# Performance work log

Measured on AMD Instinct MI355X. Metric: run time of the kernel, lower is better.

## Reference

```python
import jax, jax.numpy as jnp
import numpy as np

B, S, D, H = 4, 4096, 1024, 16
DK = D // H  # 64


def setup_inputs() -> dict:
    key = jax.random.key(0)
    ks = jax.random.split(key, 8)
    scale = 1.0 / np.sqrt(D)
    return {
        "query": jax.random.normal(ks[0], (B, S, D), dtype=jnp.float32),
        "key": jax.random.normal(ks[1], (B, S, D), dtype=jnp.float32),
        "value": jax.random.normal(ks[2], (B, S, D), dtype=jnp.float32),
        "Wq": jax.random.normal(ks[3], (D, D), dtype=jnp.float32) * scale,
        "Wk": jax.random.normal(ks[4], (D, D), dtype=jnp.float32) * scale,
        "Wv": jax.random.normal(ks[5], (D, D), dtype=jnp.float32) * scale,
        "Wo": jax.random.normal(ks[6], (D, D), dtype=jnp.float32) * scale,
        "bo": jnp.zeros((D,), dtype=jnp.float32),
    }


def _phi(x):
    # ELU + 1 feature map
    return jax.nn.elu(x) + 1.0


def _heads(x, W):
    # torch Linear: y = x @ W.T; then [B,S,D] -> [B,H,S,DK]
    y = jnp.einsum("bsd,ed->bse", x, W)
    return y.reshape(x.shape[0], x.shape[1], H, DK).transpose(0, 2, 1, 3)


def reference(query, key, value, Wq, Wk, Wv, Wo, bo):
    Q = _phi(_heads(query, Wq))   # [B,H,Sq,DK]
    K = _phi(_heads(key, Wk))     # [B,H,Sk,DK]
    V = _heads(value, Wv)         # [B,H,Sk,DK]

    KV = jnp.einsum("bhsd,bhse->bhde", K, V)        # [B,H,DK,DK]
    num = jnp.einsum("bhqd,bhde->bhqe", Q, KV)       # [B,H,Sq,DK]
    den = jnp.einsum("bhqd,bhd->bhq", Q, K.sum(axis=2))  # [B,H,Sq]
    out = num / (den[..., None] + 1e-6)

    out = out.transpose(0, 2, 1, 3).reshape(query.shape[0], query.shape[1], D)
    return jnp.einsum("bsd,ed->bse", out, Wo) + bo
```

## Files before the change

kernel.cpp:

```cpp
#include <hip/hip_runtime.h>


typedef unsigned short ushort_t;
typedef __bf16 bf16x8 __attribute__((ext_vector_type(8)));
typedef float f32x4 __attribute__((ext_vector_type(4)));
typedef void gvoid_t __attribute__((address_space(1)));
typedef void svoid_t __attribute__((address_space(3)));

#define BB 4
#define SS 4096
#define DD 1024
#define HH 16
#define DKk 64
#define MM (BB * SS)

__device__ __forceinline__ ushort_t f2bf(float f) {
  unsigned int u = __float_as_uint(f);
  u += 0x7fffu + ((u >> 16) & 1u);
  return (ushort_t)(u >> 16);
}
__device__ __forceinline__ float b2f(ushort_t h) {
  return __uint_as_float(((unsigned int)h) << 16);
}
__device__ __forceinline__ void gld_lds16(const ushort_t* g, ushort_t* l) {
  __builtin_amdgcn_global_load_lds((gvoid_t*)g, (svoid_t*)l, 16, 0, 0);
}
__device__ __forceinline__ bf16x8 ldfrag(const ushort_t* p) {
  return *(const bf16x8*)p;
}

__global__ __launch_bounds__(256) void cast3_kernel(
    const float* __restrict__ q, const float* __restrict__ k, const float* __restrict__ v,
    ushort_t* __restrict__ qd, ushort_t* __restrict__ kd, ushort_t* __restrict__ vd) {
  const int z = blockIdx.y;
  const float* s = (z == 0) ? q : (z == 1) ? k : v;
  ushort_t* d = (z == 0) ? qd : (z == 1) ? kd : vd;
  size_t i = ((size_t)blockIdx.x * 256 + threadIdx.x) * 4;
  float4 f = *(const float4*)(s + i);
  ushort4 o;
  o.x = f2bf(f.x); o.y = f2bf(f.y); o.z = f2bf(f.z); o.w = f2bf(f.w);
  *(ushort4*)(d + i) = o;
}

__global__ __launch_bounds__(256) void cast4_kernel(
    const float* __restrict__ a, const float* __restrict__ b,
    const float* __restrict__ c, const float* __restrict__ e,
    ushort_t* __restrict__ ad, ushort_t* __restrict__ bd,
    ushort_t* __restrict__ cd, ushort_t* __restrict__ ed) {
  const int z = blockIdx.y;
  const float* s = (z == 0) ? a : (z == 1) ? b : (z == 2) ? c : e;
  ushort_t* d = (z == 0) ? ad : (z == 1) ? bd : (z == 2) ? cd : ed;
  size_t i = ((size_t)blockIdx.x * 256 + threadIdx.x) * 4;
  float4 f = *(const float4*)(s + i);
  ushort4 o;
  o.x = f2bf(f.x); o.y = f2bf(f.y); o.z = f2bf(f.z); o.w = f2bf(f.w);
  *(ushort4*)(d + i) = o;
}

__global__ __launch_bounds__(256) void proj_kernel(
    const ushort_t* __restrict__ qa, const ushort_t* __restrict__ ka, const ushort_t* __restrict__ va,
    const ushort_t* __restrict__ wq, const ushort_t* __restrict__ wk, const ushort_t* __restrict__ wv,
    ushort_t* __restrict__ Qp, ushort_t* __restrict__ Kp, ushort_t* __restrict__ Vp) {
  const int z = blockIdx.z;
  const ushort_t* A = (z == 0) ? qa : (z == 1) ? ka : va;
  const ushort_t* Bw = (z == 0) ? wq : (z == 1) ? wk : wv;
  ushort_t* Y = (z == 0) ? Qp : (z == 1) ? Kp : Vp;
  const bool act = (z < 2);

  __shared__ __align__(16) ushort_t Ash[128 * 32];
  __shared__ __align__(16) ushort_t Bsh[128 * 32];
  const int t = threadIdx.x;
  const int r_ = blockIdx.x, u_ = blockIdx.y;
  const int yb = r_ + 8 * (u_ & 7) + 64 * (u_ >> 6);
  const int xb = (u_ >> 3) & 7;
  const int m0 = yb * 128, n0 = xb * 128;
  const int w = t >> 6, lane = t & 63, q4 = lane >> 4, l16 = lane & 15;
  const int wm = (w >> 1) * 64, wn = (w & 1) * 64;

  f32x4 acc[4][4];
  const f32x4 zero = {0.f, 0.f, 0.f, 0.f};
#pragma unroll
  for (int i = 0; i < 4; i++)
#pragma unroll
    for (int j = 0; j < 4; j++) acc[i][j] = zero;

  for (int k0 = 0; k0 < 1024; k0 += 32) {
#pragma unroll
    for (int it = 0; it < 2; it++) {
      int lin = it * 256 + t;
      int row = lin >> 2, ch = (lin & 3) * 8;
      gld_lds16(A + (size_t)(m0 + row) * 1024 + k0 + ch, Ash + lin * 8);
      gld_lds16(Bw + (size_t)(n0 + row) * 1024 + k0 + ch, Bsh + lin * 8);
    }
    __syncthreads();
    bf16x8 af[4], bfm[4];
#pragma unroll
    for (int mi = 0; mi < 4; mi++) af[mi] = ldfrag(&Ash[(wm + mi * 16 + l16) * 32 + q4 * 8]);
#pragma unroll
    for (int ni = 0; ni < 4; ni++) bfm[ni] = ldfrag(&Bsh[(wn + ni * 16 + l16) * 32 + q4 * 8]);
#pragma unroll
    for (int mi = 0; mi < 4; mi++)
#pragma unroll
      for (int ni = 0; ni < 4; ni++)
        acc[mi][ni] = __builtin_amdgcn_mfma_f32_16x16x32_bf16(af[mi], bfm[ni], acc[mi][ni], 0, 0, 0);
    __syncthreads();
  }
#pragma unroll
  for (int mi = 0; mi < 4; mi++)
#pragma unroll
    for (int ni = 0; ni < 4; ni++) {
      int col = n0 + wn + ni * 16 + l16;
#pragma unroll
      for (int r = 0; r < 4; r++) {
        int row = m0 + wm + mi * 16 + q4 * 4 + r;
        float vv = acc[mi][ni][r];
        if (act) vv = (vv > 0.f) ? (vv + 1.f) : __expf(vv);
        Y[(size_t)row * 1024 + col] = f2bf(vv);
      }
    }
}

__global__ __launch_bounds__(256) void out_kernel(
    const ushort_t* __restrict__ A, const ushort_t* __restrict__ Bw,
    float* __restrict__ Of, const float* __restrict__ bias) {
  __shared__ __align__(16) ushort_t Ash[128 * 32];
  __shared__ __align__(16) ushort_t Bsh[128 * 32];
  const int t = threadIdx.x;
  const int r_ = blockIdx.x, u_ = blockIdx.y;
  const int yb = r_ + 8 * (u_ & 7) + 64 * (u_ >> 6);
  const int xb = (u_ >> 3) & 7;
  const int m0 = yb * 128, n0 = xb * 128;
  const int w = t >> 6, lane = t & 63, q4 = lane >> 4, l16 = lane & 15;
  const int wm = (w >> 1) * 64, wn = (w & 1) * 64;

  f32x4 acc[4][4];
  const f32x4 zero = {0.f, 0.f, 0.f, 0.f};
#pragma unroll
  for (int i = 0; i < 4; i++)
#pragma unroll
    for (int j = 0; j < 4; j++) acc[i][j] = zero;

  for (int k0 = 0; k0 < 1024; k0 += 32) {
#pragma unroll
    for (int it = 0; it < 2; it++) {
      int lin = it * 256 + t;
      int row = lin >> 2, ch = (lin & 3) * 8;
      gld_lds16(A + (size_t)(m0 + row) * 1024 + k0 + ch, Ash + lin * 8);
      gld_lds16(Bw + (size_t)(n0 + row) * 1024 + k0 + ch, Bsh + lin * 8);
    }
    __syncthreads();
    bf16x8 af[4], bfm[4];
#pragma unroll
    for (int mi = 0; mi < 4; mi++) af[mi] = ldfrag(&Ash[(wm + mi * 16 + l16) * 32 + q4 * 8]);
#pragma unroll
    for (int ni = 0; ni < 4; ni++) bfm[ni] = ldfrag(&Bsh[(wn + ni * 16 + l16) * 32 + q4 * 8]);
#pragma unroll
    for (int mi = 0; mi < 4; mi++)
#pragma unroll
      for (int ni = 0; ni < 4; ni++)
        acc[mi][ni] = __builtin_amdgcn_mfma_f32_16x16x32_bf16(af[mi], bfm[ni], acc[mi][ni], 0, 0, 0);
    __syncthreads();
  }
#pragma unroll
  for (int mi = 0; mi < 4; mi++)
#pragma unroll
    for (int ni = 0; ni < 4; ni++) {
      int col = n0 + wn + ni * 16 + l16;
      float bv = bias[col];
#pragma unroll
      for (int r = 0; r < 4; r++) {
        int row = m0 + wm + mi * 16 + q4 * 4 + r;
        Of[(size_t)row * 1024 + col] = acc[mi][ni][r] + bv;
      }
    }
}

__global__ __launch_bounds__(256) void kv_kernel(
    const ushort_t* __restrict__ Kp, const ushort_t* __restrict__ Vp,
    float* __restrict__ KVt, float* __restrict__ Ksum) {
  const int bh = blockIdx.y, b = bh >> 4, h = bh & 15;
  const int schunk = blockIdx.x * 1024;
  const int t = threadIdx.x, w = t >> 6, lane = t & 63, q4 = lane >> 4, l16 = lane & 15;
  __shared__ ushort_t Ksh[64 * 66];
  __shared__ ushort_t Vsh[64 * 66];
  __shared__ float red[4][64];

  f32x4 acc[4];
  const f32x4 zero = {0.f, 0.f, 0.f, 0.f};
#pragma unroll
  for (int i = 0; i < 4; i++) acc[i] = zero;
  float ksum = 0.f;

  const int mat = t >> 7, tl = t & 127;
  const ushort_t* src = mat ? Vp : Kp;
  ushort_t* dsh = mat ? Vsh : Ksh;

  for (int tile = 0; tile < 16; tile++) {
    const int s0 = schunk + tile * 64;
#pragma unroll
    for (int i = 0; i < 4; i++) {
      int idx = i * 1024 + tl * 8;
      int r = idx >> 6, c = idx & 63;
      const ushort_t* g = src + (size_t)(b * 4096 + s0 + r) * 1024 + h * 64 + c;
      uint4 u = *(const uint4*)g;
      unsigned int* p = (unsigned int*)&dsh[r * 66 + c];
      p[0] = u.x; p[1] = u.y; p[2] = u.z; p[3] = u.w;
    }
    __syncthreads();
#pragma unroll
    for (int ks = 0; ks < 2; ks++) {
      ushort_t tb[8];
#pragma unroll
      for (int j = 0; j < 8; j++) tb[j] = Ksh[(ks * 32 + q4 * 8 + j) * 66 + w * 16 + l16];
      bf16x8 bfr; __builtin_memcpy(&bfr, tb, 16);
#pragma unroll
      for (int mi = 0; mi < 4; mi++) {
        ushort_t ta[8];
#pragma unroll
        for (int j = 0; j < 8; j++) ta[j] = Vsh[(ks * 32 + q4 * 8 + j) * 66 + mi * 16 + l16];
        bf16x8 afr; __builtin_memcpy(&afr, ta, 16);
        acc[mi] = __builtin_amdgcn_mfma_f32_16x16x32_bf16(afr, bfr, acc[mi], 0, 0, 0);
      }
    }
    {
      int d = t & 63;
#pragma unroll
      for (int r = 0; r < 16; r++) ksum += b2f(Ksh[((t >> 6) * 16 + r) * 66 + d]);
    }
    __syncthreads();
  }
#pragma unroll
  for (int mi = 0; mi < 4; mi++)
#pragma unroll
    for (int r = 0; r < 4; r++) {
      int e = mi * 16 + q4 * 4 + r, d = w * 16 + l16;
      atomicAdd(&KVt[(size_t)bh * 4096 + e * 64 + d], acc[mi][r]);
    }
  red[t >> 6][t & 63] = ksum;
  __syncthreads();
  if (t < 64) atomicAdd(&Ksum[bh * 64 + t], red[0][t] + red[1][t] + red[2][t] + red[3][t]);
}

__global__ __launch_bounds__(256) void num_kernel(
    const ushort_t* __restrict__ Qp, const float* __restrict__ KVt,
    const float* __restrict__ Ksum, ushort_t* __restrict__ Oc) {
  const int bh = blockIdx.y, b = bh >> 4, h = bh & 15;
  const int sblk = blockIdx.x * 256;
  const int t = threadIdx.x, w = t >> 6, lane = t & 63, q4 = lane >> 4, l16 = lane & 15;
  __shared__ __align__(16) ushort_t KVsh[64 * 72];
  __shared__ float Ks_sh[64];
  __shared__ float rden[256];

#pragma unroll
  for (int i = 0; i < 16; i++) {
    int idx = i * 256 + t;
    int e = idx >> 6, d = idx & 63;
    KVsh[e * 72 + d] = f2bf(KVt[(size_t)bh * 4096 + idx]);
  }
  if (t < 64) Ks_sh[t] = Ksum[bh * 64 + t];
  __syncthreads();

  {
    const ushort_t* qrow = Qp + (size_t)(b * 4096 + sblk + t) * 1024 + h * 64;
    float den = 1e-6f;
#pragma unroll
    for (int d = 0; d < 64; d++) den += b2f(qrow[d]) * Ks_sh[d];
    rden[t] = 1.f / den;
  }
  __syncthreads();

  f32x4 acc[4][4];
  const f32x4 zero = {0.f, 0.f, 0.f, 0.f};
#pragma unroll
  for (int i = 0; i < 4; i++)
#pragma unroll
    for (int j = 0; j < 4; j++) acc[i][j] = zero;

#pragma unroll
  for (int ks = 0; ks < 2; ks++) {
    bf16x8 af[4], bfr[4];
#pragma unroll
    for (int mi = 0; mi < 4; mi++)
      af[mi] = ldfrag(Qp + (size_t)(b * 4096 + sblk + w * 64 + mi * 16 + l16) * 1024 + h * 64 + ks * 32 + q4 * 8);
#pragma unroll
    for (int ni = 0; ni < 4; ni++)
      bfr[ni] = ldfrag(&KVsh[(ni * 16 + l16) * 72 + ks * 32 + q4 * 8]);
#pragma unroll
    for (int mi = 0; mi < 4; mi++)
#pragma unroll
      for (int ni = 0; ni < 4; ni++)
        acc[mi][ni] = __builtin_amdgcn_mfma_f32_16x16x32_bf16(af[mi], bfr[ni], acc[mi][ni], 0, 0, 0);
  }
#pragma unroll
  for (int mi = 0; mi < 4; mi++)
#pragma unroll
    for (int ni = 0; ni < 4; ni++) {
      int e = ni * 16 + l16;
#pragma unroll
      for (int r = 0; r < 4; r++) {
        int srow = w * 64 + mi * 16 + q4 * 4 + r;
        float vv = acc[mi][ni][r] * rden[srow];
        Oc[(size_t)(b * 4096 + sblk + srow) * 1024 + h * 64 + e] = f2bf(vv);
      }
    }
}

extern "C" void kernel_launch(void* const* d_in, const int* in_sizes, int n_in,
                              void* d_out, int out_size, void* d_ws, size_t ws_size,
                              hipStream_t stream) {
  const float* q  = (const float*)d_in[0];
  const float* k  = (const float*)d_in[1];
  const float* v  = (const float*)d_in[2];
  const float* Wq = (const float*)d_in[3];
  const float* Wk = (const float*)d_in[4];
  const float* Wv = (const float*)d_in[5];
  const float* Wo = (const float*)d_in[6];
  const float* bo = (const float*)d_in[7];

  char* ws = (char*)d_ws;
  const size_t SZ_IN = (size_t)MM * DD * 2;
  ushort_t* qbf = (ushort_t*)(ws);
  ushort_t* kbf = (ushort_t*)(ws + SZ_IN);
  ushort_t* vbf = (ushort_t*)(ws + 2 * SZ_IN);
  ushort_t* wqb = (ushort_t*)(ws + 3 * SZ_IN);
  ushort_t* wkb = wqb + (size_t)1024 * 1024;
  ushort_t* wvb = wkb + (size_t)1024 * 1024;
  ushort_t* wob = wvb + (size_t)1024 * 1024;
  ushort_t* Qp  = (ushort_t*)(ws + 3 * SZ_IN + 4 * (size_t)2097152);
  ushort_t* Kp  = Qp + (size_t)MM * DD;
  ushort_t* Vp  = Kp + (size_t)MM * DD;
  float* KVt    = (float*)((char*)(Vp + (size_t)MM * DD));
  float* KsumP  = KVt + (size_t)64 * 4096;
  ushort_t* Oc  = qbf;
  float* outp   = (float*)d_out;

  hipMemsetAsync(KVt, 0, ((size_t)64 * 4096 + 64 * 64) * sizeof(float), stream);
  cast3_kernel<<<dim3(16384, 3), 256, 0, stream>>>(q, k, v, qbf, kbf, vbf);
  cast4_kernel<<<dim3(1024, 4), 256, 0, stream>>>(Wq, Wk, Wv, Wo, wqb, wkb, wvb, wob);
  proj_kernel<<<dim3(8, 128, 3), 256, 0, stream>>>(qbf, kbf, vbf, wqb, wkb, wvb, Qp, Kp, Vp);
  kv_kernel<<<dim3(4, 64), 256, 0, stream>>>(Kp, Vp, KVt, KsumP);
  num_kernel<<<dim3(16, 64), 256, 0, stream>>>(Qp, KVt, KsumP, Oc);
  out_kernel<<<dim3(8, 128), 256, 0, stream>>>(Oc, wob, outp, bo);
}
```

Before: 490.3 us.

## Double-buffer LDS tiles in projection GEMMs and split KV reduction across more blocks

The projection and output GEMMs now use two LDS buffers, prefetching the next K-slice while computing on the current one. This aims to hide global load latency behind the MFMA work, at the cost of doubled shared memory per block. The KV reduction kernel uses four times as many blocks, each covering a shorter sequence chunk, to raise parallelism. The denominator computation now loads query rows with vector loads.

```diff
diff --git a/kernel.cpp b/kernel.cpp
--- a/kernel.cpp
+++ b/kernel.cpp
@@ -67,8 +67,8 @@
   ushort_t* Y = (z == 0) ? Qp : (z == 1) ? Kp : Vp;
   const bool act = (z < 2);
 
-  __shared__ __align__(16) ushort_t Ash[128 * 32];
-  __shared__ __align__(16) ushort_t Bsh[128 * 32];
+  __shared__ __align__(16) ushort_t Ash[2][128 * 32];
+  __shared__ __align__(16) ushort_t Bsh[2][128 * 32];
   const int t = threadIdx.x;
   const int r_ = blockIdx.x, u_ = blockIdx.y;
   const int yb = r_ + 8 * (u_ & 7) + 64 * (u_ >> 6);
@@ -76,6 +76,7 @@
   const int m0 = yb * 128, n0 = xb * 128;
   const int w = t >> 6, lane = t & 63, q4 = lane >> 4, l16 = lane & 15;
   const int wm = (w >> 1) * 64, wn = (w & 1) * 64;
+  const int srow = t >> 2, sch = (t & 3) * 8;
 
   f32x4 acc[4][4];
   const f32x4 zero = {0.f, 0.f, 0.f, 0.f};
@@ -84,20 +85,28 @@
 #pragma unroll
     for (int j = 0; j < 4; j++) acc[i][j] = zero;
 
-  for (int k0 = 0; k0 < 1024; k0 += 32) {
-#pragma unroll
-    for (int it = 0; it < 2; it++) {
-      int lin = it * 256 + t;
-      int row = lin >> 2, ch = (lin & 3) * 8;
-      gld_lds16(A + (size_t)(m0 + row) * 1024 + k0 + ch, Ash + lin * 8);
-      gld_lds16(Bw + (size_t)(n0 + row) * 1024 + k0 + ch, Bsh + lin * 8);
-    }
-    __syncthreads();
+  const ushort_t* ga = A + (size_t)(m0 + srow) * 1024 + sch;
+  const ushort_t* gb = Bw + (size_t)(n0 + srow) * 1024 + sch;
+
+  gld_lds16(ga + 0, &Ash[0][t * 8]);
+  gld_lds16(ga + 64 * 1024, &Ash[0][(256 + t) * 8]);
+  gld_lds16(gb + 0, &Bsh[0][t * 8]);
+  gld_lds16(gb + 64 * 1024, &Bsh[0][(256 + t) * 8]);
+  __syncthreads();
+
+  int cur = 0;
+  for (int k0 = 0; k0 < 1024; k0 += 32, cur ^= 1) {
+    if (k0 + 32 < 1024) {
+      gld_lds16(ga + (k0 + 32), &Ash[cur ^ 1][t * 8]);
+      gld_lds16(ga + (k0 + 32) + 64 * 1024, &Ash[cur ^ 1][(256 + t) * 8]);
+      gld_lds16(gb + (k0 + 32), &Bsh[cur ^ 1][t * 8]);
+      gld_lds16(gb + (k0 + 32) + 64 * 1024, &Bsh[cur ^ 1][(256 + t) * 8]);
+    }
     bf16x8 af[4], bfm[4];
 #pragma unroll
-    for (int mi = 0; mi < 4; mi++) af[mi] = ldfrag(&Ash[(wm + mi * 16 + l16) * 32 + q4 * 8]);
-#pragma unroll
-    for (int ni = 0; ni < 4; ni++) bfm[ni] = ldfrag(&Bsh[(wn + ni * 16 + l16) * 32 + q4 * 8]);
+    for (int mi = 0; mi < 4; mi++) af[mi] = ldfrag(&Ash[cur][(wm + mi * 16 + l16) * 32 + q4 * 8]);
+#pragma unroll
+    for (int ni = 0; ni < 4; ni++) bfm[ni] = ldfrag(&Bsh[cur][(wn + ni * 16 + l16) * 32 + q4 * 8]);
 #pragma unroll
     for (int mi = 0; mi < 4; mi++)
 #pragma unroll
@@ -123,8 +132,8 @@
 __global__ __launch_bounds__(256) void out_kernel(
     const ushort_t* __restrict__ A, const ushort_t* __restrict__ Bw,
     float* __restrict__ Of, const float* __restrict__ bias) {
-  __shared__ __align__(16) ushort_t Ash[128 * 32];
-  __shared__ __align__(16) ushort_t Bsh[128 * 32];
+  __shared__ __align__(16) ushort_t Ash[2][128 * 32];
+  __shared__ __align__(16) ushort_t Bsh[2][128 * 32];
   const int t = threadIdx.x;
   const int r_ = blockIdx.x, u_ = blockIdx.y;
   const int yb = r_ + 8 * (u_ & 7) + 64 * (u_ >> 6);
@@ -132,6 +141,7 @@
   const int m0 = yb * 128, n0 = xb * 128;
   const int w = t >> 6, lane = t & 63, q4 = lane >> 4, l16 = lane & 15;
   const int wm = (w >> 1) * 64, wn = (w & 1) * 64;
+  const int srow = t >> 2, sch = (t & 3) * 8;
 
   f32x4 acc[4][4];
   const f32x4 zero = {0.f, 0.f, 0.f, 0.f};
@@ -140,20 +150,28 @@
 #pragma unroll
     for (int j = 0; j < 4; j++) acc[i][j] = zero;
 
-  for (int k0 = 0; k0 < 1024; k0 += 32) {
-#pragma unroll
-    for (int it = 0; it < 2; it++) {
-      int lin = it * 256 + t;
-      int row = lin >> 2, ch = (lin & 3) * 8;
-      gld_lds16(A + (size_t)(m0 + row) * 1024 + k0 + ch, Ash + lin * 8);
-      gld_lds16(Bw + (size_t)(n0 + row) * 1024 + k0 + ch, Bsh + lin * 8);
-    }
-    __syncthreads();
+  const ushort_t* ga = A + (size_t)(m0 + srow) * 1024 + sch;
+  const ushort_t* gb = Bw + (size_t)(n0 + srow) * 1024 + sch;
+
+  gld_lds16(ga + 0, &Ash[0][t * 8]);
+  gld_lds16(ga + 64 * 1024, &Ash[0][(256 + t) * 8]);
+  gld_lds16(gb + 0, &Bsh[0][t * 8]);
+  gld_lds16(gb + 64 * 1024, &Bsh[0][(256 + t) * 8]);
+  __syncthreads();
+
+  int cur = 0;
+  for (int k0 = 0; k0 < 1024; k0 += 32, cur ^= 1) {
+    if (k0 + 32 < 1024) {
+      gld_lds16(ga + (k0 + 32), &Ash[cur ^ 1][t * 8]);
+      gld_lds16(ga + (k0 + 32) + 64 * 1024, &Ash[cur ^ 1][(256 + t) * 8]);
+      gld_lds16(gb + (k0 + 32), &Bsh[cur ^ 1][t * 8]);
+      gld_lds16(gb + (k0 + 32) + 64 * 1024, &Bsh[cur ^ 1][(256 + t) * 8]);
+    }
     bf16x8 af[4], bfm[4];
 #pragma unroll
-    for (int mi = 0; mi < 4; mi++) af[mi] = ldfrag(&Ash[(wm + mi * 16 + l16) * 32 + q4 * 8]);
-#pragma unroll
-    for (int ni = 0; ni < 4; ni++) bfm[ni] = ldfrag(&Bsh[(wn + ni * 16 + l16) * 32 + q4 * 8]);
+    for (int mi = 0; mi < 4; mi++) af[mi] = ldfrag(&Ash[cur][(wm + mi * 16 + l16) * 32 + q4 * 8]);
+#pragma unroll
+    for (int ni = 0; ni < 4; ni++) bfm[ni] = ldfrag(&Bsh[cur][(wn + ni * 16 + l16) * 32 + q4 * 8]);
 #pragma unroll
     for (int mi = 0; mi < 4; mi++)
 #pragma unroll
@@ -179,7 +197,7 @@
     const ushort_t* __restrict__ Kp, const ushort_t* __restrict__ Vp,
     float* __restrict__ KVt, float* __restrict__ Ksum) {
   const int bh = blockIdx.y, b = bh >> 4, h = bh & 15;
-  const int schunk = blockIdx.x * 1024;
+  const int schunk = blockIdx.x * 256;
   const int t = threadIdx.x, w = t >> 6, lane = t & 63, q4 = lane >> 4, l16 = lane & 15;
   __shared__ ushort_t Ksh[64 * 66];
   __shared__ ushort_t Vsh[64 * 66];
@@ -195,7 +213,7 @@
   const ushort_t* src = mat ? Vp : Kp;
   ushort_t* dsh = mat ? Vsh : Ksh;
 
-  for (int tile = 0; tile < 16; tile++) {
+  for (int tile = 0; tile < 4; tile++) {
     const int s0 = schunk + tile * 64;
 #pragma unroll
     for (int i = 0; i < 4; i++) {
@@ -264,7 +282,11 @@
     const ushort_t* qrow = Qp + (size_t)(b * 4096 + sblk + t) * 1024 + h * 64;
     float den = 1e-6f;
 #pragma unroll
-    for (int d = 0; d < 64; d++) den += b2f(qrow[d]) * Ks_sh[d];
+    for (int j = 0; j < 8; j++) {
+      bf16x8 qv = ldfrag(qrow + j * 8);
+#pragma unroll
+      for (int e = 0; e < 8; e++) den += (float)qv[e] * Ks_sh[j * 8 + e];
+    }
     rden[t] = 1.f / den;
   }
   __syncthreads();
@@ -338,7 +360,7 @@
   cast3_kernel<<<dim3(16384, 3), 256, 0, stream>>>(q, k, v, qbf, kbf, vbf);
   cast4_kernel<<<dim3(1024, 4), 256, 0, stream>>>(Wq, Wk, Wv, Wo, wqb, wkb, wvb, wob);
   proj_kernel<<<dim3(8, 128, 3), 256, 0, stream>>>(qbf, kbf, vbf, wqb, wkb, wvb, Qp, Kp, Vp);
-  kv_kernel<<<dim3(4, 64), 256, 0, stream>>>(Kp, Vp, KVt, KsumP);
+  kv_kernel<<<dim3(16, 64), 256, 0, stream>>>(Kp, Vp, KVt, KsumP);
   num_kernel<<<dim3(16, 64), 256, 0, stream>>>(Qp, KVt, KsumP, Oc);
   out_kernel<<<dim3(8, 128), 256, 0, stream>>>(Oc, wob, outp, bo);
 }
```

Result: faster. 453.2 us (-7.6%).
